# Kernel tuning notes

Measured on AMD Instinct MI355X. Metric: run time of the kernel, lower is better.

The kernel has to match this reference:

```python
import jax, jax.numpy as jnp
import numpy as np

N_ITER = 3
N_GRID = 2048
N_SENSORS = 64
N_SNAP = 128
BATCH = 128
HID = 32
VAR_NOISE = 0.1


def setup_inputs() -> dict:
    key = jax.random.key(0)
    ks = jax.random.split(key, 8)
    data = jax.random.normal(ks[0], (BATCH, N_SENSORS, N_SNAP), dtype=jnp.float32)
    A = jax.random.normal(ks[1], (N_SENSORS, N_GRID), dtype=jnp.float32)
    # per-(iteration, gridpoint) MLP: 3 -> HID -> HID -> 1 (ReLU, bias, no BN, no skip)
    s1 = 1.0 / np.sqrt(3.0)
    s2 = 1.0 / np.sqrt(HID)
    W1 = jax.random.normal(ks[2], (N_ITER, N_GRID, 3, HID), dtype=jnp.float32) * s1
    b1 = jnp.zeros((N_ITER, N_GRID, HID), dtype=jnp.float32)
    W2 = jax.random.normal(ks[3], (N_ITER, N_GRID, HID, HID), dtype=jnp.float32) * s2
    b2 = jnp.zeros((N_ITER, N_GRID, HID), dtype=jnp.float32)
    W3 = jax.random.normal(ks[4], (N_ITER, N_GRID, HID), dtype=jnp.float32) * s2
    b3 = jnp.zeros((N_ITER, N_GRID), dtype=jnp.float32)
    return {"data": data, "A": A, "W1": W1, "b1": b1, "W2": W2, "b2": b2, "W3": W3, "b3": b3}


def _iteration(g, data, A, W1, b1, W2, b2, W3, b3):
    B, m, _ = data.shape
    eye = VAR_NOISE * jnp.eye(m, dtype=data.dtype)
    # cov_yy[b] = A diag(gamma_b) A^T + var_noise I   -> [B, m, m]
    cov = jnp.einsum('bg,mg,ng->bmn', g, A, A) + eye
    t1 = jnp.linalg.solve(cov, data)                          # [B, m, T]
    t2 = jnp.linalg.solve(cov, jnp.broadcast_to(A, (B,) + A.shape))  # [B, m, G]
    T2 = jnp.abs(jnp.einsum('mg,bmg->bg', A, t2))             # diag(A^T Sigma^{-1} A)
    T1 = jnp.mean(jnp.einsum('mg,bmt->bgt', A, t1) ** 2, axis=-1)    # [B, G]
    x = jnp.stack([T1, T2, g], axis=-1)                       # [B, G, 3]
    h = jax.nn.relu(jnp.einsum('bgf,gfh->bgh', x, W1) + b1)
    h = jax.nn.relu(jnp.einsum('bgh,ghk->bgk', h, W2) + b2)
    return jnp.einsum('bgh,gh->bg', h, W3) + b3               # new gamma [B, G]


def reference(data, A, W1, b1, W2, b2, W3, b3):
    B = data.shape[0]
    g = jnp.ones((B, N_GRID), dtype=jnp.float32)
    for i in range(N_ITER):
        g = _iteration(g, data, A, W1[i], b1[i], W2[i], b2[i], W3[i], b3[i])
    return g
```

## Files before the change

### kernel.cpp

```cpp
#include <hip/hip_runtime.h>

#define NB 128
#define NM 64
#define NT 128
#define NG 2048
#define NH 32


__global__ __launch_bounds__(256) void k_init(float* __restrict__ g) {
    g[blockIdx.x * 256 + threadIdx.x] = 1.0f;
}

__global__ __launch_bounds__(256) void k_D(const float* __restrict__ data,
                                           float* __restrict__ D) {
    __shared__ float sd[64 * 133];
    int b = blockIdx.x, t = threadIdx.x;
    const float* db = data + (size_t)b * 8192;
    for (int idx = t; idx < 8192; idx += 256)
        sd[(idx >> 7) * 133 + (idx & 127)] = db[idx];
    __syncthreads();
    int i0 = (t & 15) * 4, j0 = (t >> 4) * 4;
    float acc[4][4];
#pragma unroll
    for (int r = 0; r < 4; ++r)
#pragma unroll
        for (int c = 0; c < 4; ++c) acc[r][c] = 0.f;
    for (int tt = 0; tt < 128; ++tt) {
        float av[4], bv[4];
#pragma unroll
        for (int r = 0; r < 4; ++r) av[r] = sd[(i0 + r) * 133 + tt];
#pragma unroll
        for (int c = 0; c < 4; ++c) bv[c] = sd[(j0 + c) * 133 + tt];
#pragma unroll
        for (int r = 0; r < 4; ++r)
#pragma unroll
            for (int c = 0; c < 4; ++c) acc[r][c] += av[r] * bv[c];
    }
    float* Db = D + (size_t)b * 4096;
#pragma unroll
    for (int r = 0; r < 4; ++r)
#pragma unroll
        for (int c = 0; c < 4; ++c)
            Db[(i0 + r) * 64 + j0 + c] = acc[r][c] * (1.0f / 128.0f);
}

__global__ __launch_bounds__(256) void k_cov(const float* __restrict__ A,
                                             const float* __restrict__ g,
                                             float* __restrict__ p0,
                                             float* __restrict__ p1,
                                             float* __restrict__ p2,
                                             float* __restrict__ p3) {
    int b = blockIdx.x >> 2, q = blockIdx.x & 3, t = threadIdx.x;
    int goff = q * 512;
    __shared__ float sA[32 * 64];
    __shared__ float sAg[32 * 64];
    __shared__ float sg[512];
    for (int idx = t; idx < 512; idx += 256)
        sg[idx] = g[(size_t)b * NG + goff + idx];
    float acc[4][4];
#pragma unroll
    for (int r = 0; r < 4; ++r)
#pragma unroll
        for (int c = 0; c < 4; ++c) acc[r][c] = 0.f;
    int i0 = (t & 15) * 4, j0 = (t >> 4) * 4;
    int m = t >> 2, gs = (t & 3) * 8;
    __syncthreads();
    for (int ch = 0; ch < 16; ++ch) {
        const float* Ar = A + (size_t)m * NG + goff + ch * 32 + gs;
        float4 v0 = *(const float4*)Ar;
        float4 v1 = *(const float4*)(Ar + 4);
        __syncthreads();
        sA[(gs + 0) * 64 + m] = v0.x; sAg[(gs + 0) * 64 + m] = v0.x * sg[ch * 32 + gs + 0];
        sA[(gs + 1) * 64 + m] = v0.y; sAg[(gs + 1) * 64 + m] = v0.y * sg[ch * 32 + gs + 1];
        sA[(gs + 2) * 64 + m] = v0.z; sAg[(gs + 2) * 64 + m] = v0.z * sg[ch * 32 + gs + 2];
        sA[(gs + 3) * 64 + m] = v0.w; sAg[(gs + 3) * 64 + m] = v0.w * sg[ch * 32 + gs + 3];
        sA[(gs + 4) * 64 + m] = v1.x; sAg[(gs + 4) * 64 + m] = v1.x * sg[ch * 32 + gs + 4];
        sA[(gs + 5) * 64 + m] = v1.y; sAg[(gs + 5) * 64 + m] = v1.y * sg[ch * 32 + gs + 5];
        sA[(gs + 6) * 64 + m] = v1.z; sAg[(gs + 6) * 64 + m] = v1.z * sg[ch * 32 + gs + 6];
        sA[(gs + 7) * 64 + m] = v1.w; sAg[(gs + 7) * 64 + m] = v1.w * sg[ch * 32 + gs + 7];
        __syncthreads();
#pragma unroll
        for (int gg = 0; gg < 32; ++gg) {
            float4 av = *(const float4*)&sAg[gg * 64 + i0];
            float4 bv = *(const float4*)&sA[gg * 64 + j0];
            acc[0][0] += av.x * bv.x; acc[0][1] += av.x * bv.y;
            acc[0][2] += av.x * bv.z; acc[0][3] += av.x * bv.w;
            acc[1][0] += av.y * bv.x; acc[1][1] += av.y * bv.y;
            acc[1][2] += av.y * bv.z; acc[1][3] += av.y * bv.w;
            acc[2][0] += av.z * bv.x; acc[2][1] += av.z * bv.y;
            acc[2][2] += av.z * bv.z; acc[2][3] += av.z * bv.w;
            acc[3][0] += av.w * bv.x; acc[3][1] += av.w * bv.y;
            acc[3][2] += av.w * bv.z; acc[3][3] += av.w * bv.w;
        }
    }
    float* dst = (q == 0 ? p0 : q == 1 ? p1 : q == 2 ? p2 : p3) + (size_t)b * 4096;
#pragma unroll
    for (int r = 0; r < 4; ++r)
#pragma unroll
        for (int c = 0; c < 4; ++c)
            dst[(i0 + r) * 64 + j0 + c] = acc[r][c];
}

#define GJSTEP(RB, WB, KK)                                                    \
    {                                                                         \
        const float* krow = (RB) + (KK) * 68;                                 \
        const float* rowp = (RB) + lane * 68;                                 \
        float4 prow[16], own[16];                                             \
        _Pragma("unroll")                                                     \
        for (int bj = 0; bj < 16; ++bj) prow[bj] = *(const float4*)(krow + 4 * bj); \
        _Pragma("unroll")                                                     \
        for (int bj = 0; bj < 16; ++bj) own[bj] = *(const float4*)(rowp + 4 * bj);  \
        float p = krow[KK];                                                   \
        float c = rowp[KK];                                                   \
        float ps = (__builtin_fabsf(p) < 1e-12f) ? (p >= 0.f ? 1e-12f : -1e-12f) : p; \
        float pinv = __builtin_amdgcn_rcpf(ps);                               \
        bool isk = (lane == (KK));                                            \
        float n  = isk ? 0.0f : 1.0f;                                         \
        float m2 = isk ? -pinv : c * pinv;                                    \
        float* wr = (WB) + lane * 68;                                         \
        _Pragma("unroll")                                                     \
        for (int bj = 0; bj < 16; ++bj) {                                     \
            float4 res;                                                       \
            res.x = own[bj].x * n - m2 * prow[bj].x;                          \
            res.y = own[bj].y * n - m2 * prow[bj].y;                          \
            res.z = own[bj].z * n - m2 * prow[bj].z;                          \
            res.w = own[bj].w * n - m2 * prow[bj].w;                          \
            *(float4*)(wr + 4 * bj) = res;                                    \
        }                                                                     \
        wr[KK] = isk ? pinv : -m2;   \
    }

#define GEMMT(Ash, Bsh)                                                       \
    {                                                                         \
        _Pragma("unroll")                                                     \
        for (int rr = 0; rr < 4; ++rr)                                        \
            for (int cc = 0; cc < 4; ++cc) acc[rr][cc] = 0.f;                 \
        _Pragma("unroll 4")                                                   \
        for (int kk = 0; kk < 64; kk += 4) {                                  \
            float4 av[4], bv[4];                                              \
            _Pragma("unroll")                                                 \
            for (int qq = 0; qq < 4; ++qq) {                                  \
                av[qq] = *(const float4*)((Ash) + (kk + qq) * 68 + i0);       \
                bv[qq] = *(const float4*)((Bsh) + (kk + qq) * 68 + j0);       \
            }                                                                 \
            _Pragma("unroll")                                                 \
            for (int qq = 0; qq < 4; ++qq) {                                  \
                acc[0][0] += av[qq].x * bv[qq].x; acc[0][1] += av[qq].x * bv[qq].y; \
                acc[0][2] += av[qq].x * bv[qq].z; acc[0][3] += av[qq].x * bv[qq].w; \
                acc[1][0] += av[qq].y * bv[qq].x; acc[1][1] += av[qq].y * bv[qq].y; \
                acc[1][2] += av[qq].y * bv[qq].z; acc[1][3] += av[qq].y * bv[qq].w; \
                acc[2][0] += av[qq].z * bv[qq].x; acc[2][1] += av[qq].z * bv[qq].y; \
                acc[2][2] += av[qq].z * bv[qq].z; acc[2][3] += av[qq].z * bv[qq].w; \
                acc[3][0] += av[qq].w * bv[qq].x; acc[3][1] += av[qq].w * bv[qq].y; \
                acc[3][2] += av[qq].w * bv[qq].z; acc[3][3] += av[qq].w * bv[qq].w; \
            }                                                                 \
        }                                                                     \
    }

__global__ __launch_bounds__(256, 1) void k_invpost(const float* p0, const float* p1,
                                                    const float* p2, const float* p3,
                                                    const float* Dws,
                                                    float* Sbuf, float* Mbuf) {
    __shared__ float sX[64 * 68];
    __shared__ float sA[64 * 68];
    __shared__ float sR[64 * 68];
    int t = threadIdx.x, b = blockIdx.x;
    size_t boff = (size_t)b * 4096;

    float4 dreg[4];
#pragma unroll
    for (int u = 0; u < 4; ++u)
        dreg[u] = ((const float4*)(Dws + boff))[u * 256 + t];

#pragma unroll
    for (int u = 0; u < 4; ++u) {
        int idx = u * 1024 + t * 4;
        int i = idx >> 6, j = idx & 63;
        float4 v0 = *(const float4*)(p0 + boff + idx);
        float4 v1 = *(const float4*)(p1 + boff + idx);
        float4 v2 = *(const float4*)(p2 + boff + idx);
        float4 v3 = *(const float4*)(p3 + boff + idx);
        float4 v = make_float4((v0.x + v1.x) + (v2.x + v3.x),
                               (v0.y + v1.y) + (v2.y + v3.y),
                               (v0.z + v1.z) + (v2.z + v3.z),
                               (v0.w + v1.w) + (v2.w + v3.w));
        int d = i - j;
        if (d >= 0 && d < 4) (&v.x)[d] += 0.1f;
        *(float4*)(sX + i * 68 + j) = v;
        *(float4*)(sA + i * 68 + j) = v;
    }
    __syncthreads();

    if (t < 64) {
        int lane = t;
#pragma unroll 1
        for (int k2 = 0; k2 < 32; ++k2) {
            GJSTEP(sX, sR, 2 * k2);
            GJSTEP(sR, sX, 2 * k2 + 1);
        }
    }
    __syncthreads();

    int i0 = (t & 15) * 4, j0 = (t >> 4) * 4;
    float acc[4][4];

    GEMMT(sA, sX);
#pragma unroll
    for (int rr = 0; rr < 4; ++rr)
#pragma unroll
        for (int cc = 0; cc < 4; ++cc)
            sR[(i0 + rr) * 68 + j0 + cc] =
                ((i0 + rr) == (j0 + cc) ? 2.0f : 0.0f) - acc[rr][cc];
    __syncthreads();

    GEMMT(sX, sR);
#pragma unroll
    for (int rr = 0; rr < 4; ++rr) {
#pragma unroll
        for (int cc = 0; cc < 4; ++cc)
            sA[(i0 + rr) * 68 + j0 + cc] = acc[rr][cc];
        *(float4*)(Sbuf + boff + (i0 + rr) * 64 + j0) =
            make_float4(acc[rr][0], acc[rr][1], acc[rr][2], acc[rr][3]);
    }
    __syncthreads();

#pragma unroll
    for (int u = 0; u < 4; ++u) {
        int idx = u * 1024 + t * 4;
        *(float4*)(sX + (idx >> 6) * 68 + (idx & 63)) = dreg[u];
    }
    __syncthreads();

    GEMMT(sX, sA);
    __syncthreads();
#pragma unroll
    for (int rr = 0; rr < 4; ++rr)
#pragma unroll
        for (int cc = 0; cc < 4; ++cc)
            sR[(i0 + rr) * 68 + j0 + cc] = acc[rr][cc];
    __syncthreads();

    GEMMT(sA, sR);
#pragma unroll
    for (int rr = 0; rr < 4; ++rr)
        *(float4*)(Mbuf + boff + (i0 + rr) * 64 + j0) =
            make_float4(acc[rr][0], acc[rr][1], acc[rr][2], acc[rr][3]);
}

__global__ __launch_bounds__(256, 1) void k_feat(const float* __restrict__ A,
                                                 const float* __restrict__ Sbuf,
                                                 const float* __restrict__ Mbuf,
                                                 float* __restrict__ T1,
                                                 float* __restrict__ T2) {
    __shared__ float sS[4096];
    __shared__ float sM[4096];
    __shared__ float sa[4096];
    int t = threadIdx.x;
    int b = blockIdx.x >> 3, tile = blockIdx.x & 7;
    const float* Abase = A + tile * 256;
    {
        const float4* S4 = (const float4*)(Sbuf + (size_t)b * 4096);
        const float4* M4 = (const float4*)(Mbuf + (size_t)b * 4096);
#pragma unroll
        for (int u = 0; u < 4; ++u) {
            ((float4*)sS)[u * 256 + t] = S4[u * 256 + t];
            ((float4*)sM)[u * 256 + t] = M4[u * 256 + t];
        }
#pragma unroll
        for (int u = 0; u < 4; ++u) {
            int idx = u * 1024 + t * 4;
            int kk = idx >> 8, gl = idx & 255;
            *(float4*)(sa + idx) = *(const float4*)(Abase + (size_t)kk * NG + gl);
        }
    }
    int iq = t >> 4, gq = t & 15;
    int i0 = iq * 4;
    float accS[4][16], accM[4][16];
#pragma unroll
    for (int r = 0; r < 4; ++r)
#pragma unroll
        for (int c = 0; c < 16; ++c) { accS[r][c] = 0.f; accM[r][c] = 0.f; }
    __syncthreads();

#pragma unroll 1
    for (int p = 0; p < 4; ++p) {
        if (p) {
            __syncthreads();
#pragma unroll
            for (int u = 0; u < 4; ++u) {
                int idx = u * 1024 + t * 4;
                int kk = idx >> 8, gl = idx & 255;
                *(float4*)(sa + idx) =
                    *(const float4*)(Abase + (size_t)(p * 16 + kk) * NG + gl);
            }
            __syncthreads();
        }
#pragma unroll 2
        for (int kk = 0; kk < 16; ++kk) {
            int k = p * 16 + kk;
            float4 sf = *(const float4*)(sS + k * 64 + i0);
            float4 mf = *(const float4*)(sM + k * 64 + i0);
            const float* ak = sa + kk * 256 + gq * 4;
            float4 a0 = *(const float4*)(ak);
            float4 a1 = *(const float4*)(ak + 64);
            float4 a2 = *(const float4*)(ak + 128);
            float4 a3 = *(const float4*)(ak + 192);
            float af[16] = {a0.x, a0.y, a0.z, a0.w, a1.x, a1.y, a1.z, a1.w,
                            a2.x, a2.y, a2.z, a2.w, a3.x, a3.y, a3.z, a3.w};
#pragma unroll
            for (int r = 0; r < 4; ++r) {
                float sr = (&sf.x)[r];
                float mr = (&mf.x)[r];
#pragma unroll
                for (int c = 0; c < 16; ++c) {
                    accS[r][c] += sr * af[c];
                    accM[r][c] += mr * af[c];
                }
            }
        }
    }

    float pS[16], pM[16];
#pragma unroll
    for (int c = 0; c < 16; ++c) { pS[c] = 0.f; pM[c] = 0.f; }
#pragma unroll
    for (int r = 0; r < 4; ++r) {
        const float* arp = A + (size_t)(i0 + r) * NG + tile * 256 + gq * 4;
        float4 b0 = *(const float4*)(arp);
        float4 b1 = *(const float4*)(arp + 64);
        float4 b2 = *(const float4*)(arp + 128);
        float4 b3 = *(const float4*)(arp + 192);
        float ar[16] = {b0.x, b0.y, b0.z, b0.w, b1.x, b1.y, b1.z, b1.w,
                        b2.x, b2.y, b2.z, b2.w, b3.x, b3.y, b3.z, b3.w};
#pragma unroll
        for (int c = 0; c < 16; ++c) {
            pS[c] += ar[c] * accS[r][c];
            pM[c] += ar[c] * accM[r][c];
        }
    }
    __syncthreads();

#pragma unroll
    for (int ch = 0; ch < 4; ++ch) {
        *(float4*)(sS + iq * 256 + ch * 64 + gq * 4) =
            make_float4(pS[ch * 4], pS[ch * 4 + 1], pS[ch * 4 + 2], pS[ch * 4 + 3]);
        *(float4*)(sM + iq * 256 + ch * 64 + gq * 4) =
            make_float4(pM[ch * 4], pM[ch * 4 + 1], pM[ch * 4 + 2], pM[ch * 4 + 3]);
    }
    __syncthreads();

    float sumS = 0.f, sumM = 0.f;
#pragma unroll
    for (int q = 0; q < 16; ++q) {
        sumS += sS[q * 256 + t];
        sumM += sM[q * 256 + t];
    }
    size_t base = (size_t)b * NG + tile * 256 + t;
    T2[base] = fabsf(sumS);
    T1[base] = sumM;
}

__global__ __launch_bounds__(256, 1) void k_mlp(const float* __restrict__ T1,
                                                const float* __restrict__ T2,
                                                const float* __restrict__ gcur,
                                                const float* __restrict__ W1,
                                                const float* __restrict__ b1,
                                                const float* __restrict__ W2,
                                                const float* __restrict__ b2,
                                                const float* __restrict__ W3,
                                                const float* __restrict__ b3,
                                                int it, float* __restrict__ out) {
    __shared__ float w[9896];
    int t = threadIdx.x, g0 = blockIdx.x * 8;
    {
        size_t gbase = (size_t)it * NG + g0;
        const float* srcW1 = W1 + gbase * 96;
        const float* srcB1 = b1 + gbase * 32;
        const float* srcW2 = W2 + gbase * 1024;
        const float* srcB2 = b2 + gbase * 32;
        const float* srcW3 = W3 + gbase * 32;
        const float* srcB3 = b3 + gbase;
#pragma unroll
        for (int u = 0; u < 8; ++u)
            *(float4*)(w + 1088 + u * 1028 + t * 4) =
                ((const float4*)srcW2)[u * 256 + t];
        if (t < 192) {
            int gl = t / 24, j4 = t % 24;
            *(float4*)(w + gl * 100 + j4 * 4) = ((const float4*)srcW1)[t];
        } else {
            int i = t - 192, gl = i >> 3, j4 = i & 7;
            *(float4*)(w + 800 + gl * 36 + j4 * 4) = ((const float4*)srcB1)[i];
        }
        if (t < 64) {
            int gl = t >> 3, j4 = t & 7;
            *(float4*)(w + 9312 + gl * 36 + j4 * 4) = ((const float4*)srcB2)[t];
        } else if (t < 128) {
            int i = t - 64, gl = i >> 3, j4 = i & 7;
            *(float4*)(w + 9600 + gl * 36 + j4 * 4) = ((const float4*)srcW3)[i];
        } else if (t < 136) {
            w[9888 + (t - 128)] = srcB3[t - 128];
        }
    }
    __syncthreads();
    int gl = t & 7, gg = g0 + gl;
    const float* w1d = w + gl * 100;
    const float* b1d = w + 800 + gl * 36;
    const float* w2d = w + 1088 + gl * 1028;
    const float* b2d = w + 9312 + gl * 36;
    const float* w3d = w + 9600 + gl * 36;
    float b3v = w[9888 + gl];
    int b0 = t >> 3;

    float x0[4], x1[4], x2[4];
#pragma unroll
    for (int c = 0; c < 4; ++c) {
        size_t xo = (size_t)(b0 + c * 32) * NG + gg;
        x0[c] = T1[xo]; x1[c] = T2[xo]; x2[c] = gcur[xo];
    }

    float h1[4][32];
#pragma unroll
    for (int k = 0; k < 32; k += 4) {
        float4 wa = *(const float4*)(w1d + k);
        float4 wb = *(const float4*)(w1d + 32 + k);
        float4 wc = *(const float4*)(w1d + 64 + k);
        float4 bv = *(const float4*)(b1d + k);
#pragma unroll
        for (int c = 0; c < 4; ++c) {
            h1[c][k + 0] = fmaxf(0.f, x0[c] * wa.x + x1[c] * wb.x + x2[c] * wc.x + bv.x);
            h1[c][k + 1] = fmaxf(0.f, x0[c] * wa.y + x1[c] * wb.y + x2[c] * wc.y + bv.y);
            h1[c][k + 2] = fmaxf(0.f, x0[c] * wa.z + x1[c] * wb.z + x2[c] * wc.z + bv.z);
            h1[c][k + 3] = fmaxf(0.f, x0[c] * wa.w + x1[c] * wb.w + x2[c] * wc.w + bv.w);
        }
    }

    float acc[4];
#pragma unroll
    for (int c = 0; c < 4; ++c) acc[c] = b3v;
#pragma unroll 1
    for (int k = 0; k < 32; k += 4) {
        float4 hb = *(const float4*)(b2d + k);
        float v[4][4];
#pragma unroll
        for (int c = 0; c < 4; ++c) {
            v[c][0] = hb.x; v[c][1] = hb.y; v[c][2] = hb.z; v[c][3] = hb.w;
        }
#pragma unroll
        for (int j = 0; j < 32; ++j) {
            float4 w2v = *(const float4*)(w2d + j * 32 + k);
#pragma unroll
            for (int c = 0; c < 4; ++c) {
                v[c][0] += h1[c][j] * w2v.x;
                v[c][1] += h1[c][j] * w2v.y;
                v[c][2] += h1[c][j] * w2v.z;
                v[c][3] += h1[c][j] * w2v.w;
            }
        }
        float4 w3v = *(const float4*)(w3d + k);
#pragma unroll
        for (int c = 0; c < 4; ++c) {
            acc[c] += fmaxf(0.f, v[c][0]) * w3v.x + fmaxf(0.f, v[c][1]) * w3v.y +
                      fmaxf(0.f, v[c][2]) * w3v.z + fmaxf(0.f, v[c][3]) * w3v.w;
        }
    }
#pragma unroll
    for (int c = 0; c < 4; ++c)
        out[(size_t)(b0 + c * 32) * NG + gg] = acc[c];
}

extern "C" void kernel_launch(void* const* d_in, const int* in_sizes, int n_in,
                              void* d_out, int out_size, void* d_ws, size_t ws_size,
                              hipStream_t stream) {
    const float* data = (const float*)d_in[0];
    const float* A    = (const float*)d_in[1];
    const float* W1   = (const float*)d_in[2];
    const float* b1   = (const float*)d_in[3];
    const float* W2   = (const float*)d_in[4];
    const float* b2   = (const float*)d_in[5];
    const float* W3   = (const float*)d_in[6];
    const float* b3   = (const float*)d_in[7];
    float* out = (float*)d_out;
    float* ws = (float*)d_ws;

    float* D  = ws;
    float* P0 = ws + 524288;
    float* P1 = ws + 1048576;
    float* P2 = ws + 1572864;
    float* P3 = ws + 2097152;
    float* T1 = ws + 2621440;
    float* T2 = ws + 2883584;
    float* gA = ws + 3145728;
    float* gB = ws + 3407872;

    k_init<<<dim3(1024), dim3(256), 0, stream>>>(gA);
    k_D<<<dim3(128), dim3(256), 0, stream>>>(data, D);

    float* gc = gA;
    float* gn = gB;
    for (int it = 0; it < 3; ++it) {
        k_cov<<<dim3(512), dim3(256), 0, stream>>>(A, gc, P0, P1, P2, P3);
        k_invpost<<<dim3(128), dim3(256), 0, stream>>>(P0, P1, P2, P3, D, P0, P1);
        k_feat<<<dim3(1024), dim3(256), 0, stream>>>(A, P0, P1, T1, T2);
        float* dst = (it == 2) ? out : gn;
        k_mlp<<<dim3(256), dim3(256), 0, stream>>>(T1, T2, gc, W1, b1, W2, b2, W3, b3, it, dst);
        float* tmp = gc; gc = gn; gn = tmp;
    }
}
```

Measured before the change: 563.5 us.

## Use 8x8 register tiles with split-K across waves in covariance kernel

The covariance-partial kernel now computes a full 64x64 output tile per wave using 8x8 register blocks. The grid dimension is split across the four waves, and partial sums are reduced through shared memory with a tree reduction. Staging chunks double to 64 grid points, which halves the number of sync rounds and raises the FMA-to-LDS-load ratio. In exchange it uses more registers (64 accumulators), adds reduction syncs, and leaves only one wave doing the final store.

```diff
diff --git a/kernel.cpp b/kernel.cpp
--- a/kernel.cpp
+++ b/kernel.cpp
@@ -52,53 +52,92 @@
                                              float* __restrict__ p3) {
     int b = blockIdx.x >> 2, q = blockIdx.x & 3, t = threadIdx.x;
     int goff = q * 512;
-    __shared__ float sA[32 * 64];
-    __shared__ float sAg[32 * 64];
+    __shared__ float sA[64 * 64];
+    __shared__ float sAg[64 * 64];
     __shared__ float sg[512];
     for (int idx = t; idx < 512; idx += 256)
         sg[idx] = g[(size_t)b * NG + goff + idx];
-    float acc[4][4];
-#pragma unroll
-    for (int r = 0; r < 4; ++r)
-#pragma unroll
-        for (int c = 0; c < 4; ++c) acc[r][c] = 0.f;
-    int i0 = (t & 15) * 4, j0 = (t >> 4) * 4;
-    int m = t >> 2, gs = (t & 3) * 8;
-    __syncthreads();
-    for (int ch = 0; ch < 16; ++ch) {
-        const float* Ar = A + (size_t)m * NG + goff + ch * 32 + gs;
+    float acc[8][8];
+#pragma unroll
+    for (int r = 0; r < 8; ++r)
+#pragma unroll
+        for (int c = 0; c < 8; ++c) acc[r][c] = 0.f;
+    int w = t >> 6, l = t & 63;
+    int i0 = (l & 7) * 8, j0 = (l >> 3) * 8;
+    int m = t >> 2, gs = (t & 3) * 16;
+
+#pragma unroll 1
+    for (int rd = 0; rd < 8; ++rd) {
+        const float* Ar = A + (size_t)m * NG + goff + rd * 64 + gs;
         float4 v0 = *(const float4*)Ar;
         float4 v1 = *(const float4*)(Ar + 4);
+        float4 v2 = *(const float4*)(Ar + 8);
+        float4 v3 = *(const float4*)(Ar + 12);
         __syncthreads();
-        sA[(gs + 0) * 64 + m] = v0.x; sAg[(gs + 0) * 64 + m] = v0.x * sg[ch * 32 + gs + 0];
-        sA[(gs + 1) * 64 + m] = v0.y; sAg[(gs + 1) * 64 + m] = v0.y * sg[ch * 32 + gs + 1];
-        sA[(gs + 2) * 64 + m] = v0.z; sAg[(gs + 2) * 64 + m] = v0.z * sg[ch * 32 + gs + 2];
-        sA[(gs + 3) * 64 + m] = v0.w; sAg[(gs + 3) * 64 + m] = v0.w * sg[ch * 32 + gs + 3];
-        sA[(gs + 4) * 64 + m] = v1.x; sAg[(gs + 4) * 64 + m] = v1.x * sg[ch * 32 + gs + 4];
-        sA[(gs + 5) * 64 + m] = v1.y; sAg[(gs + 5) * 64 + m] = v1.y * sg[ch * 32 + gs + 5];
-        sA[(gs + 6) * 64 + m] = v1.z; sAg[(gs + 6) * 64 + m] = v1.z * sg[ch * 32 + gs + 6];
-        sA[(gs + 7) * 64 + m] = v1.w; sAg[(gs + 7) * 64 + m] = v1.w * sg[ch * 32 + gs + 7];
+        {
+            const float* sgr = sg + rd * 64 + gs;
+            float vv[16] = {v0.x, v0.y, v0.z, v0.w, v1.x, v1.y, v1.z, v1.w,
+                            v2.x, v2.y, v2.z, v2.w, v3.x, v3.y, v3.z, v3.w};
+#pragma unroll
+            for (int u = 0; u < 16; ++u) {
+                sA[(gs + u) * 64 + m] = vv[u];
+                sAg[(gs + u) * 64 + m] = vv[u] * sgr[u];
+            }
+        }
         __syncthreads();
-#pragma unroll
-        for (int gg = 0; gg < 32; ++gg) {
-            float4 av = *(const float4*)&sAg[gg * 64 + i0];
-            float4 bv = *(const float4*)&sA[gg * 64 + j0];
-            acc[0][0] += av.x * bv.x; acc[0][1] += av.x * bv.y;
-            acc[0][2] += av.x * bv.z; acc[0][3] += av.x * bv.w;
-            acc[1][0] += av.y * bv.x; acc[1][1] += av.y * bv.y;
-            acc[1][2] += av.y * bv.z; acc[1][3] += av.y * bv.w;
-            acc[2][0] += av.z * bv.x; acc[2][1] += av.z * bv.y;
-            acc[2][2] += av.z * bv.z; acc[2][3] += av.z * bv.w;
-            acc[3][0] += av.w * bv.x; acc[3][1] += av.w * bv.y;
-            acc[3][2] += av.w * bv.z; acc[3][3] += av.w * bv.w;
-        }
-    }
-    float* dst = (q == 0 ? p0 : q == 1 ? p1 : q == 2 ? p2 : p3) + (size_t)b * 4096;
-#pragma unroll
-    for (int r = 0; r < 4; ++r)
-#pragma unroll
-        for (int c = 0; c < 4; ++c)
-            dst[(i0 + r) * 64 + j0 + c] = acc[r][c];
+#pragma unroll 4
+        for (int u = 0; u < 16; ++u) {
+            int gg = w * 16 + u;
+            const float* avp = sAg + gg * 64 + i0;
+            const float* bvp = sA + gg * 64 + j0;
+            float4 a0 = *(const float4*)avp;
+            float4 a1 = *(const float4*)(avp + 4);
+            float4 bb0 = *(const float4*)bvp;
+            float4 bb1 = *(const float4*)(bvp + 4);
+            float av[8] = {a0.x, a0.y, a0.z, a0.w, a1.x, a1.y, a1.z, a1.w};
+            float bv[8] = {bb0.x, bb0.y, bb0.z, bb0.w, bb1.x, bb1.y, bb1.z, bb1.w};
+#pragma unroll
+            for (int r = 0; r < 8; ++r)
+#pragma unroll
+                for (int c = 0; c < 8; ++c)
+                    acc[r][c] += av[r] * bv[c];
+        }
+    }
+
+    __syncthreads();
+    if (w == 1) {
+#pragma unroll
+        for (int j = 0; j < 64; ++j) sA[j * 64 + l] = acc[j >> 3][j & 7];
+    } else if (w == 3) {
+#pragma unroll
+        for (int j = 0; j < 64; ++j) sAg[j * 64 + l] = acc[j >> 3][j & 7];
+    }
+    __syncthreads();
+    if (w == 0) {
+#pragma unroll
+        for (int j = 0; j < 64; ++j) acc[j >> 3][j & 7] += sA[j * 64 + l];
+    } else if (w == 2) {
+#pragma unroll
+        for (int j = 0; j < 64; ++j) acc[j >> 3][j & 7] += sAg[j * 64 + l];
+    }
+    __syncthreads();
+    if (w == 2) {
+#pragma unroll
+        for (int j = 0; j < 64; ++j) sA[j * 64 + l] = acc[j >> 3][j & 7];
+    }
+    __syncthreads();
+    if (w == 0) {
+#pragma unroll
+        for (int j = 0; j < 64; ++j) acc[j >> 3][j & 7] += sA[j * 64 + l];
+        float* dst = (q == 0 ? p0 : q == 1 ? p1 : q == 2 ? p2 : p3) + (size_t)b * 4096;
+#pragma unroll
+        for (int r = 0; r < 8; ++r) {
+            *(float4*)(dst + (i0 + r) * 64 + j0) =
+                make_float4(acc[r][0], acc[r][1], acc[r][2], acc[r][3]);
+            *(float4*)(dst + (i0 + r) * 64 + j0 + 4) =
+                make_float4(acc[r][4], acc[r][5], acc[r][6], acc[r][7]);
+        }
+    }
 }
 
 #define GJSTEP(RB, WB, KK)                                                    \
```

After: 558.4 us. Within noise of the previous version (-0.9%).
